# Kernel optimization log

Measured on AMD Instinct MI355X. Metric: run time of the kernel, lower is better.

## Reference

```python
import jax, jax.numpy as jnp
import numpy as np

N = 100000      # num nodes (cells)
M = 100000      # num hyperedges (hyperedge_attr has N rows, so M <= N; torch code uses max(idx1)+1)
NNZ = 3200000   # incidence entries
C = 10          # num_of_class
D_IN = 64
HID = 512


def setup_inputs() -> dict:
    key = jax.random.key(0)
    ks = jax.random.split(key, 16)
    s = 0.05
    return {
        "embedding": jax.random.normal(ks[0], (N, D_IN), jnp.float32),
        "edge_index": jax.random.randint(ks[1], (2, NNZ), 0, N, jnp.int32),
        "hyperedge_attr": jax.random.normal(ks[2], (N, D_IN), jnp.float32),
        "wq": jax.random.normal(ks[3], (D_IN, HID), jnp.float32) * s,
        "bq": jnp.zeros((HID,), jnp.float32),
        "wk": jax.random.normal(ks[4], (D_IN, HID), jnp.float32) * s,
        "bk": jnp.zeros((HID,), jnp.float32),
        "wv": jax.random.normal(ks[5], (D_IN, HID), jnp.float32) * s,
        "bv": jnp.zeros((HID,), jnp.float32),
        "wo": jax.random.normal(ks[6], (HID, D_IN), jnp.float32) * s,
        "bo": jnp.zeros((D_IN,), jnp.float32),
        "hconv_lin": jax.random.normal(ks[7], (D_IN, 1), jnp.float32) * s,
        "hconv_att": jax.random.normal(ks[8], (1, 1, 2), jnp.float32) * s,
        "hconv_bias": jnp.zeros((1,), jnp.float32),
        "head_lin": jax.random.normal(ks[9], (1, 1), jnp.float32) * s,
        "head_bias": jnp.zeros((1,), jnp.float32),
        "out_w": jax.random.normal(ks[10], (1, C), jnp.float32) * s,
        "out_b": jnp.zeros((C,), jnp.float32),
    }


def reference(embedding, edge_index, hyperedge_attr, wq, bq, wk, bk, wv, bv,
              wo, bo, hconv_lin, hconv_att, hconv_bias, head_lin, head_bias,
              out_w, out_b):
    n = embedding.shape[0]
    nnz = edge_index.shape[1]

    # ---- DualAttention over per-node sequences of length 1 ----
    x1 = embedding[:, None, :]        # [N,1,64]
    x2 = hyperedge_attr[:, None, :]   # [N,1,64]

    def sdpa(x):  # self-attention with shared Q/K/V projections
        Q = x @ wq + bq
        K = x @ wk + bk
        V = x @ wv + bv
        scores = jnp.einsum('nsd,ntd->nst', Q, K) / jnp.sqrt(jnp.float32(HID))
        return jnp.einsum('nst,ntd->nsd', jax.nn.softmax(scores, axis=-1), V)

    att_out = (sdpa(x1) + sdpa(x2)) @ wo + bo  # [N,1,64]

    idx0 = edge_index[0]  # node ids per incidence
    idx1 = edge_index[1]  # hyperedge ids per incidence

    # degree normalizations (hyperedge_weight = ones)
    ones_e = jnp.ones((nnz,), jnp.float32)
    Bdeg = jax.ops.segment_sum(ones_e, idx1, num_segments=M)  # edge size
    Binv = jnp.where(Bdeg > 0, 1.0 / Bdeg, 0.0)
    Ddeg = jax.ops.segment_sum(ones_e, idx0, num_segments=n)  # node degree
    Dinv = jnp.where(Ddeg > 0, 1.0 / Ddeg, 0.0)

    def hconv_propagate(xnode, alpha):
        # xnode: [N,H,F]; node -> edge then edge -> node, with degree norms
        m1 = Binv[idx1][:, None, None] * xnode[idx0]
        if alpha is not None:
            m1 = alpha[:, :, None] * m1
        ef = jax.ops.segment_sum(m1, idx1, num_segments=M)     # [M,H,F]
        m2 = Dinv[idx0][:, None, None] * ef[idx1]
        if alpha is not None:
            m2 = alpha[:, :, None] * m2
        return jax.ops.segment_sum(m2, idx0, num_segments=n)   # [N,H,F]

    # ---- HypergraphConv(64,1, use_attention=True), heads=1, out=1 ----
    xl = jnp.einsum('nsd,df->nsf', att_out, hconv_lin)            # [N,1,1]
    el = (hyperedge_attr @ hconv_lin)[:, :, None]                 # [N,1,1]
    alpha = (xl[idx0][:, :, 0] * hconv_att[0, :, 0] +
             el[idx1][:, :, 0] * hconv_att[0, :, 1])              # [nnz,1]
    alpha = jax.nn.leaky_relu(alpha, 0.2)
    # softmax grouped by hyperedge id (attention_mode='node')
    amax = jax.ops.segment_max(alpha, idx1, num_segments=M)
    aexp = jnp.exp(alpha - amax[idx1])
    asum = jax.ops.segment_sum(aexp, idx1, num_segments=M)
    alpha = aexp / asum[idx1]

    h = hconv_propagate(xl, alpha).reshape(n, 1) + hconv_bias     # [N,1]

    # ---- head conv: HypergraphConv(1,1), no attention ----
    hl = (h @ head_lin)[:, :, None]                               # [N,1,1]
    out = hconv_propagate(hl, None).reshape(n, 1) + head_bias     # [N,1]

    emb = jax.nn.relu(out)
    return emb @ out_w + out_b                                    # [N,C]
```

## Files before the change

### kernel.cpp

```cpp
#include <hip/hip_runtime.h>

#define M_SEG    100000
#define LOCW     256
#define LOG_LOCW 8
#define CAP      8832
#define NBS      391
#define NBT      782
#define BINB     512
#define BINT     512
#define CAPR     16
#define NROUND   2

#define FPS  4398046511104.f
#define FPSI 2.2737367544323206e-13

typedef float v4f __attribute__((ext_vector_type(4)));

__device__ __forceinline__ float edge_e(float xv, float ev, float a0, float a1) {
    float a = xv * a0 + ev * a1;
    a = a > 0.f ? a : 0.2f * a;
    return __expf(a);
}

__device__ __forceinline__ void fxadd(unsigned long long* p, float v) {
    atomicAdd(p, (unsigned long long)(long long)(v * FPS));
}
__device__ __forceinline__ float fxget(unsigned long long v) {
    return (float)((double)(long long)v * FPSI);
}

__global__ void prep_kernel(const float* __restrict__ wv, const float* __restrict__ bv,
                            const float* __restrict__ wo, const float* __restrict__ bo,
                            const float* __restrict__ hlin,
                            float* __restrict__ w_eff, float* __restrict__ c_eff) {
    __shared__ float wol[512];
    __shared__ float hl_s[64];
    __shared__ float part[512];
    __shared__ float cpart[512];
    int t = threadIdx.x;
    if (t < 64) hl_s[t] = hlin[t];
    __syncthreads();
    {
        float s = 0.f;
        for (int j = 0; j < 64; ++j) s += wo[t * 64 + j] * hl_s[j];
        wol[t] = s;
    }
    __syncthreads();
    {
        int d = t & 63, kseg = t >> 6;
        float s = 0.f;
        for (int k = kseg * 64; k < kseg * 64 + 64; ++k) s += wv[d * 512 + k] * wol[k];
        part[t] = s;
        float cs = 0.f;
        for (int k = kseg * 64; k < kseg * 64 + 64; ++k) cs += 2.f * bv[k] * wol[k];
        cpart[t] = cs;
    }
    __syncthreads();
    if (t < 64) {
        float s = 0.f;
        for (int r = 0; r < 8; ++r) s += part[r * 64 + t];
        w_eff[t] = s;
    }
    if (t == 64) {
        float s = 0.f;
        for (int r = 0; r < 512; ++r) s += cpart[r];
        for (int j = 0; j < 64; ++j) s += bo[j] * hl_s[j];
        *c_eff = s;
    }
}

__global__ void node1_kernel(const v4f* __restrict__ emb, const v4f* __restrict__ hattr,
                             const v4f* __restrict__ w_eff4, const v4f* __restrict__ hlin4,
                             const float* __restrict__ c_eff,
                             float* __restrict__ xl, float* __restrict__ el, int n) {
    int gtid = blockIdx.x * blockDim.x + threadIdx.x;
    int wave = gtid >> 6;
    int lane = threadIdx.x & 63;
    int sub  = lane >> 4;
    int q    = lane & 15;
    int node = wave * 4 + sub;
    if (node >= n) return;
    size_t base = (size_t)node * 16 + q;
    v4f ha = __builtin_nontemporal_load(hattr + base);
    v4f em = __builtin_nontemporal_load(emb + base);
    v4f w  = w_eff4[q];
    v4f h  = hlin4[q];
    float v1 = (em[0] + ha[0]) * w[0] + (em[1] + ha[1]) * w[1] +
               (em[2] + ha[2]) * w[2] + (em[3] + ha[3]) * w[3];
    float v2 = ha[0] * h[0] + ha[1] * h[1] + ha[2] * h[2] + ha[3] * h[3];
    for (int off = 8; off >= 1; off >>= 1) {
        v1 += __shfl_xor(v1, off);
        v2 += __shfl_xor(v2, off);
    }
    if (q == 0) { xl[node] = v1 + *c_eff; el[node] = v2; }
}

__global__ void hist_kernel(const int* __restrict__ idx0, const int* __restrict__ idx1,
                            unsigned* __restrict__ hist, long long nnz) {
    __shared__ unsigned h[NBT];
    for (int i = threadIdx.x; i < NBT; i += BINT) h[i] = 0u;
    __syncthreads();
    long long chunk = (nnz + BINB - 1) / BINB;
    long long e0 = (long long)blockIdx.x * chunk;
    long long e1 = e0 + chunk; if (e1 > nnz) e1 = nnz;
    for (long long e = e0 + threadIdx.x; e < e1; e += BINT) {
        int i1 = __builtin_nontemporal_load(idx1 + e);
        int i0 = __builtin_nontemporal_load(idx0 + e);
        atomicAdd(&h[i1 >> LOG_LOCW], 1u);
        atomicAdd(&h[NBS + (i0 >> LOG_LOCW)], 1u);
    }
    __syncthreads();
    for (int i = threadIdx.x; i < NBT; i += BINT)
        hist[(size_t)i * BINB + blockIdx.x] = h[i];
}

__global__ void scan_kernel(const unsigned* __restrict__ hist, unsigned* __restrict__ offs,
                            unsigned* __restrict__ cnt) {
    int gb = blockIdx.x;
    int lane = threadIdx.x;
    unsigned running = 0;
    unsigned base = (unsigned)gb * CAP;
    for (int c = 0; c < BINB; c += 64) {
        unsigned v = hist[(size_t)gb * BINB + c + lane];
        unsigned s = v;
        for (int off = 1; off < 64; off <<= 1) {
            unsigned t = __shfl_up(s, off);
            if (lane >= off) s += t;
        }
        offs[(size_t)gb * BINB + c + lane] = base + running + (s - v);
        running += __shfl(s, 63);
    }
    if (lane == 0) cnt[gb] = running;
}

__global__ void scat_kernel(const int* __restrict__ idx0, const int* __restrict__ idx1,
                            const unsigned* __restrict__ offs,
                            unsigned* __restrict__ recs, long long nnz) {
    __shared__ unsigned base_s[NBT];
    __shared__ unsigned cum_s[NBT];
    __shared__ unsigned alloc_s[NBT];
    __shared__ unsigned stage[NBT][CAPR];
    for (int i = threadIdx.x; i < NBT; i += BINT) {
        base_s[i] = offs[(size_t)i * BINB + blockIdx.x];
        cum_s[i]  = 0u;
    }
    long long chunk = (nnz + BINB - 1) / BINB;
    long long e0 = (long long)blockIdx.x * chunk;
    long long e1 = e0 + chunk; if (e1 > nnz) e1 = nnz;
    long long rchunk = (chunk + NROUND - 1) / NROUND;

    for (int rd = 0; rd < NROUND; ++rd) {
        __syncthreads();
        for (int i = threadIdx.x; i < NBT; i += BINT) alloc_s[i] = 0u;
        __syncthreads();
        long long r0 = e0 + (long long)rd * rchunk;
        long long r1 = r0 + rchunk; if (r1 > e1) r1 = e1;
        long long e = r0 + threadIdx.x;
        for (; e + 3LL * BINT < r1; e += 4LL * BINT) {
            int i0v[4], i1v[4];
            #pragma unroll
            for (int u = 0; u < 4; ++u) {
                i0v[u] = __builtin_nontemporal_load(idx0 + e + (long long)u * BINT);
                i1v[u] = __builtin_nontemporal_load(idx1 + e + (long long)u * BINT);
            }
            #pragma unroll
            for (int u = 0; u < 4; ++u) {
                int i0 = i0v[u], i1 = i1v[u];
                {
                    int b = i1 >> LOG_LOCW;
                    unsigned rec = ((unsigned)i0 << LOG_LOCW) | (unsigned)(i1 & (LOCW - 1));
                    unsigned s = atomicAdd(&alloc_s[b], 1u);
                    if (s < CAPR) stage[b][s] = rec;
                    else {
                        unsigned pos = base_s[b] + cum_s[b] + s;
                        if (pos < (unsigned)(b + 1) * CAP) recs[pos] = rec;
                    }
                }
                {
                    int b = NBS + (i0 >> LOG_LOCW);
                    unsigned rec = ((unsigned)i1 << LOG_LOCW) | (unsigned)(i0 & (LOCW - 1));
                    unsigned s = atomicAdd(&alloc_s[b], 1u);
                    if (s < CAPR) stage[b][s] = rec;
                    else {
                        unsigned pos = base_s[b] + cum_s[b] + s;
                        if (pos < (unsigned)(b + 1) * CAP) recs[pos] = rec;
                    }
                }
            }
        }
        for (; e < r1; e += BINT) {
            int i0 = __builtin_nontemporal_load(idx0 + e);
            int i1 = __builtin_nontemporal_load(idx1 + e);
            {
                int b = i1 >> LOG_LOCW;
                unsigned rec = ((unsigned)i0 << LOG_LOCW) | (unsigned)(i1 & (LOCW - 1));
                unsigned s = atomicAdd(&alloc_s[b], 1u);
                if (s < CAPR) stage[b][s] = rec;
                else {
                    unsigned pos = base_s[b] + cum_s[b] + s;
                    if (pos < (unsigned)(b + 1) * CAP) recs[pos] = rec;
                }
            }
            {
                int b = NBS + (i0 >> LOG_LOCW);
                unsigned rec = ((unsigned)i1 << LOG_LOCW) | (unsigned)(i0 & (LOCW - 1));
                unsigned s = atomicAdd(&alloc_s[b], 1u);
                if (s < CAPR) stage[b][s] = rec;
                else {
                    unsigned pos = base_s[b] + cum_s[b] + s;
                    if (pos < (unsigned)(b + 1) * CAP) recs[pos] = rec;
                }
            }
        }
        __syncthreads();
        {
            int r = threadIdx.x & (CAPR - 1);
            for (int b = threadIdx.x / CAPR; b < NBT; b += BINT / CAPR) {
                unsigned a = alloc_s[b]; if (a > CAPR) a = CAPR;
                if (r < a) {
                    unsigned pos = base_s[b] + cum_s[b] + r;
                    if (pos < (unsigned)(b + 1) * CAP) recs[pos] = stage[b][r];
                }
            }
        }
        __syncthreads();
        for (int i = threadIdx.x; i < NBT; i += BINT) cum_s[i] += alloc_s[i];
    }
}

__global__ void p1r_kernel(const unsigned* __restrict__ recs, const unsigned* __restrict__ cnt,
                           const float* __restrict__ xl, const float* __restrict__ el,
                           const float* __restrict__ hatt,
                           float* __restrict__ Binv, float2* __restrict__ elt2, int m_tot) {
    int b = blockIdx.x;
    __shared__ unsigned long long As[LOCW], Ex[LOCW];
    __shared__ unsigned Bc[LOCW];
    __shared__ float el_loc[LOCW];
    int t = threadIdx.x;
    if (t < LOCW) {
        As[t] = 0ull; Ex[t] = 0ull; Bc[t] = 0u;
        int m = (b << LOG_LOCW) + t;
        el_loc[t] = (m < m_tot) ? el[m] : 0.f;
    }
    __syncthreads();
    float a0 = hatt[0], a1 = hatt[1];
    unsigned c = cnt[b]; if (c > CAP) c = CAP;
    const unsigned* bp = recs + (size_t)b * CAP;
    unsigned k = t;
    for (; k + 7u * 512u < c; k += 8u * 512u) {
        unsigned r[8]; float xv[8];
        #pragma unroll
        for (int u = 0; u < 8; ++u) r[u] = bp[k + u * 512u];
        #pragma unroll
        for (int u = 0; u < 8; ++u) xv[u] = xl[r[u] >> LOG_LOCW];
        #pragma unroll
        for (int u = 0; u < 8; ++u) {
            int l = r[u] & (LOCW - 1);
            float ee = edge_e(xv[u], el_loc[l], a0, a1);
            fxadd(&As[l], ee);
            fxadd(&Ex[l], ee * xv[u]);
            atomicAdd(&Bc[l], 1u);
        }
    }
    for (; k < c; k += 512u) {
        unsigned rec = bp[k];
        int l = rec & (LOCW - 1);
        float xv = xl[rec >> LOG_LOCW];
        float ee = edge_e(xv, el_loc[l], a0, a1);
        fxadd(&As[l], ee);
        fxadd(&Ex[l], ee * xv);
        atomicAdd(&Bc[l], 1u);
    }
    __syncthreads();
    if (t < LOCW) {
        int m = (b << LOG_LOCW) + t;
        if (m < m_tot) {
            unsigned bd = Bc[t];
            float as = fxget(As[t]);
            float ex = fxget(Ex[t]);
            Binv[m] = bd ? 1.f / (float)bd : 0.f;
            float tv = bd ? ex / ((float)bd * as * as) : 0.f;
            elt2[m] = make_float2(el_loc[t], tv);
        }
    }
}

__global__ void p2r_kernel(const unsigned* __restrict__ recs, const unsigned* __restrict__ cnt,
                           const float* __restrict__ xl, const float2* __restrict__ elt2,
                           const float* __restrict__ hatt,
                           const float* __restrict__ hbias, const float* __restrict__ headlin,
                           float* __restrict__ hl, float* __restrict__ Dinv, int n) {
    int b = blockIdx.x;
    int gb = NBS + b;
    __shared__ unsigned long long Hs[LOCW];
    __shared__ unsigned Dc[LOCW];
    __shared__ float xl_loc[LOCW];
    int t = threadIdx.x;
    if (t < LOCW) {
        Hs[t] = 0ull; Dc[t] = 0u;
        int i = (b << LOG_LOCW) + t;
        xl_loc[t] = (i < n) ? xl[i] : 0.f;
    }
    __syncthreads();
    float a0 = hatt[0], a1 = hatt[1];
    unsigned c = cnt[gb]; if (c > CAP) c = CAP;
    const unsigned* bp = recs + (size_t)gb * CAP;
    unsigned k = t;
    for (; k + 7u * 512u < c; k += 8u * 512u) {
        unsigned r[8]; float2 et[8];
        #pragma unroll
        for (int u = 0; u < 8; ++u) r[u] = bp[k + u * 512u];
        #pragma unroll
        for (int u = 0; u < 8; ++u) et[u] = elt2[r[u] >> LOG_LOCW];
        #pragma unroll
        for (int u = 0; u < 8; ++u) {
            int l = r[u] & (LOCW - 1);
            float ee = edge_e(xl_loc[l], et[u].x, a0, a1);
            fxadd(&Hs[l], ee * et[u].y);
            atomicAdd(&Dc[l], 1u);
        }
    }
    for (; k < c; k += 512u) {
        unsigned rec = bp[k];
        int l = rec & (LOCW - 1);
        float2 et = elt2[rec >> LOG_LOCW];
        float ee = edge_e(xl_loc[l], et.x, a0, a1);
        fxadd(&Hs[l], ee * et.y);
        atomicAdd(&Dc[l], 1u);
    }
    __syncthreads();
    if (t < LOCW) {
        int i = (b << LOG_LOCW) + t;
        if (i < n) {
            unsigned dd = Dc[t];
            float dinv = dd ? 1.f / (float)dd : 0.f;
            Dinv[i] = dinv;
            hl[i] = (dinv * fxget(Hs[t]) + hbias[0]) * headlin[0];
        }
    }
}

__global__ void p3r_kernel(const unsigned* __restrict__ recs, const unsigned* __restrict__ cnt,
                           const float* __restrict__ hl, const float* __restrict__ Binv,
                           float* __restrict__ ef2b, int m_tot) {
    int b = blockIdx.x;
    __shared__ unsigned long long Es[LOCW];
    int t = threadIdx.x;
    if (t < LOCW) Es[t] = 0ull;
    __syncthreads();
    unsigned c = cnt[b]; if (c > CAP) c = CAP;
    const unsigned* bp = recs + (size_t)b * CAP;
    unsigned k = t;
    for (; k + 7u * 512u < c; k += 8u * 512u) {
        unsigned r[8]; float hv[8];
        #pragma unroll
        for (int u = 0; u < 8; ++u) r[u] = bp[k + u * 512u];
        #pragma unroll
        for (int u = 0; u < 8; ++u) hv[u] = hl[r[u] >> LOG_LOCW];
        #pragma unroll
        for (int u = 0; u < 8; ++u) fxadd(&Es[r[u] & (LOCW - 1)], hv[u]);
    }
    for (; k < c; k += 512u) {
        unsigned rec = bp[k];
        fxadd(&Es[rec & (LOCW - 1)], hl[rec >> LOG_LOCW]);
    }
    __syncthreads();
    if (t < LOCW) {
        int m = (b << LOG_LOCW) + t;
        if (m < m_tot) ef2b[m] = fxget(Es[t]) * Binv[m];
    }
}

__global__ void p4r_kernel(const unsigned* __restrict__ recs, const unsigned* __restrict__ cnt,
                           const float* __restrict__ ef2b, const float* __restrict__ Dinv,
                           const float* __restrict__ headbias,
                           const float* __restrict__ out_w, const float* __restrict__ out_b,
                           float* __restrict__ out, int n, int C) {
    int b = blockIdx.x;
    int gb = NBS + b;
    __shared__ unsigned long long Os[LOCW];
    __shared__ float r_loc[LOCW];
    int t = threadIdx.x;
    if (t < LOCW) Os[t] = 0ull;
    __syncthreads();
    unsigned c = cnt[gb]; if (c > CAP) c = CAP;
    const unsigned* bp = recs + (size_t)gb * CAP;
    unsigned k = t;
    for (; k + 7u * 512u < c; k += 8u * 512u) {
        unsigned r[8]; float ev[8];
        #pragma unroll
        for (int u = 0; u < 8; ++u) r[u] = bp[k + u * 512u];
        #pragma unroll
        for (int u = 0; u < 8; ++u) ev[u] = ef2b[r[u] >> LOG_LOCW];
        #pragma unroll
        for (int u = 0; u < 8; ++u) fxadd(&Os[r[u] & (LOCW - 1)], ev[u]);
    }
    for (; k < c; k += 512u) {
        unsigned rec = bp[k];
        fxadd(&Os[rec & (LOCW - 1)], ef2b[rec >> LOG_LOCW]);
    }
    __syncthreads();
    if (t < LOCW) {
        int i = (b << LOG_LOCW) + t;
        float o = (i < n) ? Dinv[i] * fxget(Os[t]) + headbias[0] : 0.f;
        r_loc[t] = o > 0.f ? o : 0.f;
    }
    __syncthreads();
    int total = LOCW * C;
    for (int idx = t; idx < total; idx += 512) {
        int il = idx / C, cc = idx - il * C;
        int i = (b << LOG_LOCW) + il;
        if (i < n) out[(size_t)i * C + cc] = r_loc[il] * out_w[cc] + out_b[cc];
    }
}

__global__ void f_node1(const float* __restrict__ emb, const float* __restrict__ hattr,
                        const float* __restrict__ w_eff, const float* __restrict__ hlin,
                        const float* __restrict__ c_eff,
                        float* __restrict__ xl, float* __restrict__ el, int n) {
    int wid = (int)((blockIdx.x * (long long)blockDim.x + threadIdx.x) >> 6);
    int lane = threadIdx.x & 63;
    if (wid >= n) return;
    size_t base = (size_t)wid * 64 + lane;
    float ha = hattr[base];
    float eh = emb[base] + ha;
    float v1 = eh * w_eff[lane];
    float v2 = ha * hlin[lane];
    for (int off = 32; off > 0; off >>= 1) {
        v1 += __shfl_xor(v1, off);
        v2 += __shfl_xor(v2, off);
    }
    if (lane == 0) { xl[wid] = v1 + *c_eff; el[wid] = v2; }
}
__global__ void f_p1(const int* __restrict__ idx0, const int* __restrict__ idx1,
                     const float* __restrict__ xl, const float* __restrict__ el,
                     const float* __restrict__ hatt,
                     float* __restrict__ B, float* __restrict__ D,
                     float* __restrict__ A, float* __restrict__ E, long long nnz) {
    float a0 = hatt[0], a1 = hatt[1];
    long long stride = (long long)gridDim.x * blockDim.x;
    for (long long e = blockIdx.x * (long long)blockDim.x + threadIdx.x; e < nnz; e += stride) {
        int i0 = idx0[e], i1 = idx1[e];
        float xv = xl[i0];
        float ee = edge_e(xv, el[i1], a0, a1);
        atomicAdd(&B[i1], 1.f); atomicAdd(&D[i0], 1.f);
        atomicAdd(&A[i1], ee);  atomicAdd(&E[i1], ee * xv);
    }
}
__global__ void f_r1m(const float* __restrict__ B, const float* __restrict__ A,
                      const float* __restrict__ E,
                      float* __restrict__ Binv, float* __restrict__ t, int m) {
    int i = blockIdx.x * blockDim.x + threadIdx.x;
    if (i >= m) return;
    float bd = B[i];
    Binv[i] = bd > 0.f ? 1.f / bd : 0.f;
    t[i]    = bd > 0.f ? E[i] / (bd * A[i] * A[i]) : 0.f;
}
__global__ void f_r1n(const float* __restrict__ D, float* __restrict__ Dinv, int n) {
    int i = blockIdx.x * blockDim.x + threadIdx.x;
    if (i < n) { float dd = D[i]; Dinv[i] = dd > 0.f ? 1.f / dd : 0.f; }
}
__global__ void f_p2(const int* __restrict__ idx0, const int* __restrict__ idx1,
                     const float* __restrict__ xl, const float* __restrict__ el,
                     const float* __restrict__ hatt, const float* __restrict__ t,
                     float* __restrict__ H, long long nnz) {
    float a0 = hatt[0], a1 = hatt[1];
    long long stride = (long long)gridDim.x * blockDim.x;
    for (long long e = blockIdx.x * (long long)blockDim.x + threadIdx.x; e < nnz; e += stride) {
        int i0 = idx0[e], i1 = idx1[e];
        float ee = edge_e(xl[i0], el[i1], a0, a1);
        atomicAdd(&H[i0], ee * t[i1]);
    }
}
__global__ void f_r2(const float* __restrict__ H, const float* __restrict__ Dinv,
                     const float* __restrict__ hbias, const float* __restrict__ headlin,
                     float* __restrict__ hl, int n) {
    int i = blockIdx.x * blockDim.x + threadIdx.x;
    if (i < n) hl[i] = (Dinv[i] * H[i] + hbias[0]) * headlin[0];
}
__global__ void f_p3(const int* __restrict__ idx0, const int* __restrict__ idx1,
                     const float* __restrict__ hl, float* __restrict__ E2, long long nnz) {
    long long stride = (long long)gridDim.x * blockDim.x;
    for (long long e = blockIdx.x * (long long)blockDim.x + threadIdx.x; e < nnz; e += stride)
        atomicAdd(&E2[idx1[e]], hl[idx0[e]]);
}
__global__ void f_r3(const float* __restrict__ E2, const float* __restrict__ Binv,
                     float* __restrict__ ef2b, int m) {
    int i = blockIdx.x * blockDim.x + threadIdx.x;
    if (i < m) ef2b[i] = E2[i] * Binv[i];
}
__global__ void f_p4(const int* __restrict__ idx0, const int* __restrict__ idx1,
                     const float* __restrict__ ef2b, float* __restrict__ O, long long nnz) {
    long long stride = (long long)gridDim.x * blockDim.x;
    for (long long e = blockIdx.x * (long long)blockDim.x + threadIdx.x; e < nnz; e += stride)
        atomicAdd(&O[idx0[e]], ef2b[idx1[e]]);
}
__global__ void f_out(const float* __restrict__ O, const float* __restrict__ Dinv,
                      const float* __restrict__ headbias,
                      const float* __restrict__ out_w, const float* __restrict__ out_b,
                      float* __restrict__ out, int n, int C) {
    int i = blockIdx.x * blockDim.x + threadIdx.x;
    if (i >= n) return;
    float o = Dinv[i] * O[i] + headbias[0];
    float r = o > 0.f ? o : 0.f;
    for (int c = 0; c < C; ++c) out[(size_t)i * C + c] = r * out_w[c] + out_b[c];
}

extern "C" void kernel_launch(void* const* d_in, const int* in_sizes, int n_in,
                              void* d_out, int out_size, void* d_ws, size_t ws_size,
                              hipStream_t stream) {
    const float* emb     = (const float*)d_in[0];
    const int*   eidx    = (const int*)  d_in[1];
    const float* hattr   = (const float*)d_in[2];
    const float* wv      = (const float*)d_in[7];
    const float* bv      = (const float*)d_in[8];
    const float* wo      = (const float*)d_in[9];
    const float* bo      = (const float*)d_in[10];
    const float* hlin    = (const float*)d_in[11];
    const float* hatt    = (const float*)d_in[12];
    const float* hbias   = (const float*)d_in[13];
    const float* headlin = (const float*)d_in[14];
    const float* headbias= (const float*)d_in[15];
    const float* out_w   = (const float*)d_in[16];
    const float* out_b   = (const float*)d_in[17];

    int n = in_sizes[0] / 64;
    long long nnz = in_sizes[1] / 2;
    int C = in_sizes[16];
    const int M = M_SEG;
    const int* idx0 = eidx;
    const int* idx1 = eidx + nnz;

    size_t need_words = 2 * (size_t)NBT * BINB
                      + NBT
                      + (size_t)NBT * CAP
                      + 8 * (size_t)n + 80;
    bool ok = (ws_size >= need_words * sizeof(unsigned)) && (n == 100000);

    float* ws = (float*)d_ws;

    if (ok) {
        unsigned* hist = (unsigned*)ws;
        unsigned* offs = hist + (size_t)NBT * BINB;
        unsigned* cnt  = offs + (size_t)NBT * BINB;
        unsigned* recs = cnt + NBT;
        float2* elt2 = (float2*)(recs + (size_t)NBT * CAP);
        float* xl    = (float*)(elt2 + n);
        float* el    = xl + n;
        float* Binv  = el + n;
        float* Dinv  = Binv + M;
        float* hl    = Dinv + n;
        float* ef2b  = hl + n;
        float* w_eff = ef2b + M;
        float* c_eff = w_eff + 64;

        prep_kernel<<<1, 512, 0, stream>>>(wv, bv, wo, bo, hlin, w_eff, c_eff);
        int n1_blocks = ((n + 3) / 4 + 3) / 4;
        node1_kernel<<<n1_blocks, 256, 0, stream>>>((const v4f*)emb, (const v4f*)hattr,
                                                    (const v4f*)w_eff, (const v4f*)hlin,
                                                    c_eff, xl, el, n);

        hist_kernel<<<BINB, BINT, 0, stream>>>(idx0, idx1, hist, nnz);
        scan_kernel<<<NBT, 64, 0, stream>>>(hist, offs, cnt);
        scat_kernel<<<BINB, BINT, 0, stream>>>(idx0, idx1, offs, recs, nnz);

        p1r_kernel<<<NBS, 512, 0, stream>>>(recs, cnt, xl, el, hatt, Binv, elt2, M);
        p2r_kernel<<<NBS, 512, 0, stream>>>(recs, cnt, xl, elt2, hatt, hbias, headlin,
                                            hl, Dinv, n);
        p3r_kernel<<<NBS, 512, 0, stream>>>(recs, cnt, hl, Binv, ef2b, M);
        p4r_kernel<<<NBS, 512, 0, stream>>>(recs, cnt, ef2b, Dinv, headbias, out_w, out_b,
                                            (float*)d_out, n, C);
    } else {
        float* B    = ws;
        float* D    = B + M;
        float* A    = D + n;
        float* E    = A + M;
        float* H    = E + M;
        float* E2   = H + n;
        float* O    = E2 + M;
        float* zend = O + n;
        float* xl    = zend;
        float* el    = xl + n;
        float* Binv  = el + n;
        float* tbuf  = Binv + M;
        float* Dinv  = tbuf + M;
        float* hl    = Dinv + n;
        float* ef2b  = hl + n;
        float* w_eff = ef2b + M;
        float* c_eff = w_eff + 64;

        hipMemsetAsync(d_ws, 0, (size_t)(zend - ws) * sizeof(float), stream);
        prep_kernel<<<1, 512, 0, stream>>>(wv, bv, wo, bo, hlin, w_eff, c_eff);
        f_node1<<<(n + 3) / 4, 256, 0, stream>>>(emb, hattr, w_eff, hlin, c_eff, xl, el, n);

        const int EG = 2048, EB = 256;
        int mg = (M + 255) / 256, ng = (n + 255) / 256;
        f_p1<<<EG, EB, 0, stream>>>(idx0, idx1, xl, el, hatt, B, D, A, E, nnz);
        f_r1m<<<mg, 256, 0, stream>>>(B, A, E, Binv, tbuf, M);
        f_r1n<<<ng, 256, 0, stream>>>(D, Dinv, n);
        f_p2<<<EG, EB, 0, stream>>>(idx0, idx1, xl, el, hatt, tbuf, H, nnz);
        f_r2<<<ng, 256, 0, stream>>>(H, Dinv, hbias, headlin, hl, n);
        f_p3<<<EG, EB, 0, stream>>>(idx0, idx1, hl, E2, nnz);
        f_r3<<<mg, 256, 0, stream>>>(E2, Binv, ef2b, M);
        f_p4<<<EG, EB, 0, stream>>>(idx0, idx1, ef2b, O, nnz);
        f_out<<<ng, 256, 0, stream>>>(O, Dinv, headbias, out_w, out_b, (float*)d_out, n, C);
    }
}
```

Baseline: 157.9 us.

## Merge launch pairs and pack degree counts into fixed-point LDS atomics

Fuses the weight-prep kernel into the histogram launch as an extra block, and fuses the node projection with the per-bucket scan into one launch, removing two kernel launches and their serialization gaps. In p1r and p2r the separate degree-count LDS atomic is removed: the count is packed into the top 12 bits of the 64-bit fixed-point accumulator, using 41 fractional bits and adding a +2 bias for signed values in p2r. This halves LDS atomics in those passes but narrows fixed-point range and precision, and caps the per-slot count field at 4095.

```diff
diff --git a/kernel.cpp b/kernel.cpp
--- a/kernel.cpp
+++ b/kernel.cpp
@@ -11,8 +11,12 @@
 #define CAPR     16
 #define NROUND   2
 
-#define FPS  4398046511104.f
-#define FPSI 2.2737367544323206e-13
+#define FPS42  4398046511104.f
+#define FPSI42 2.2737367544323206e-13
+#define FPS41  2199023255552.f
+#define FPSI41 4.547473508864641e-13
+#define MASK52 ((1ULL << 52) - 1ULL)
+#define CNT1   (1ULL << 52)
 
 typedef float v4f __attribute__((ext_vector_type(4)));
 
@@ -22,115 +26,118 @@
     return __expf(a);
 }
 
-__device__ __forceinline__ void fxadd(unsigned long long* p, float v) {
-    atomicAdd(p, (unsigned long long)(long long)(v * FPS));
-}
-__device__ __forceinline__ float fxget(unsigned long long v) {
-    return (float)((double)(long long)v * FPSI);
-}
-
-__global__ void prep_kernel(const float* __restrict__ wv, const float* __restrict__ bv,
-                            const float* __restrict__ wo, const float* __restrict__ bo,
-                            const float* __restrict__ hlin,
-                            float* __restrict__ w_eff, float* __restrict__ c_eff) {
+__device__ __forceinline__ void fxadd42(unsigned long long* p, float v) {
+    atomicAdd(p, (unsigned long long)(long long)(v * FPS42));
+}
+__device__ __forceinline__ float fxget42(unsigned long long v) {
+    return (float)((double)(long long)v * FPSI42);
+}
+
+__global__ void histprep_kernel(const int* __restrict__ idx0, const int* __restrict__ idx1,
+                                unsigned* __restrict__ hist, long long nnz,
+                                const float* __restrict__ wv, const float* __restrict__ bv,
+                                const float* __restrict__ wo, const float* __restrict__ bo,
+                                const float* __restrict__ hlin,
+                                float* __restrict__ w_eff, float* __restrict__ c_eff) {
+    __shared__ unsigned h[NBT];
     __shared__ float wol[512];
     __shared__ float hl_s[64];
     __shared__ float part[512];
     __shared__ float cpart[512];
     int t = threadIdx.x;
-    if (t < 64) hl_s[t] = hlin[t];
-    __syncthreads();
-    {
-        float s = 0.f;
-        for (int j = 0; j < 64; ++j) s += wo[t * 64 + j] * hl_s[j];
-        wol[t] = s;
-    }
-    __syncthreads();
-    {
-        int d = t & 63, kseg = t >> 6;
-        float s = 0.f;
-        for (int k = kseg * 64; k < kseg * 64 + 64; ++k) s += wv[d * 512 + k] * wol[k];
-        part[t] = s;
-        float cs = 0.f;
-        for (int k = kseg * 64; k < kseg * 64 + 64; ++k) cs += 2.f * bv[k] * wol[k];
-        cpart[t] = cs;
-    }
-    __syncthreads();
-    if (t < 64) {
-        float s = 0.f;
-        for (int r = 0; r < 8; ++r) s += part[r * 64 + t];
-        w_eff[t] = s;
-    }
-    if (t == 64) {
-        float s = 0.f;
-        for (int r = 0; r < 512; ++r) s += cpart[r];
-        for (int j = 0; j < 64; ++j) s += bo[j] * hl_s[j];
-        *c_eff = s;
-    }
-}
-
-__global__ void node1_kernel(const v4f* __restrict__ emb, const v4f* __restrict__ hattr,
-                             const v4f* __restrict__ w_eff4, const v4f* __restrict__ hlin4,
-                             const float* __restrict__ c_eff,
-                             float* __restrict__ xl, float* __restrict__ el, int n) {
-    int gtid = blockIdx.x * blockDim.x + threadIdx.x;
-    int wave = gtid >> 6;
-    int lane = threadIdx.x & 63;
-    int sub  = lane >> 4;
-    int q    = lane & 15;
-    int node = wave * 4 + sub;
-    if (node >= n) return;
-    size_t base = (size_t)node * 16 + q;
-    v4f ha = __builtin_nontemporal_load(hattr + base);
-    v4f em = __builtin_nontemporal_load(emb + base);
-    v4f w  = w_eff4[q];
-    v4f h  = hlin4[q];
-    float v1 = (em[0] + ha[0]) * w[0] + (em[1] + ha[1]) * w[1] +
-               (em[2] + ha[2]) * w[2] + (em[3] + ha[3]) * w[3];
-    float v2 = ha[0] * h[0] + ha[1] * h[1] + ha[2] * h[2] + ha[3] * h[3];
-    for (int off = 8; off >= 1; off >>= 1) {
-        v1 += __shfl_xor(v1, off);
-        v2 += __shfl_xor(v2, off);
-    }
-    if (q == 0) { xl[node] = v1 + *c_eff; el[node] = v2; }
-}
-
-__global__ void hist_kernel(const int* __restrict__ idx0, const int* __restrict__ idx1,
-                            unsigned* __restrict__ hist, long long nnz) {
-    __shared__ unsigned h[NBT];
-    for (int i = threadIdx.x; i < NBT; i += BINT) h[i] = 0u;
-    __syncthreads();
-    long long chunk = (nnz + BINB - 1) / BINB;
-    long long e0 = (long long)blockIdx.x * chunk;
-    long long e1 = e0 + chunk; if (e1 > nnz) e1 = nnz;
-    for (long long e = e0 + threadIdx.x; e < e1; e += BINT) {
-        int i1 = __builtin_nontemporal_load(idx1 + e);
-        int i0 = __builtin_nontemporal_load(idx0 + e);
-        atomicAdd(&h[i1 >> LOG_LOCW], 1u);
-        atomicAdd(&h[NBS + (i0 >> LOG_LOCW)], 1u);
-    }
-    __syncthreads();
-    for (int i = threadIdx.x; i < NBT; i += BINT)
-        hist[(size_t)i * BINB + blockIdx.x] = h[i];
-}
-
-__global__ void scan_kernel(const unsigned* __restrict__ hist, unsigned* __restrict__ offs,
-                            unsigned* __restrict__ cnt) {
-    int gb = blockIdx.x;
-    int lane = threadIdx.x;
-    unsigned running = 0;
-    unsigned base = (unsigned)gb * CAP;
-    for (int c = 0; c < BINB; c += 64) {
-        unsigned v = hist[(size_t)gb * BINB + c + lane];
-        unsigned s = v;
-        for (int off = 1; off < 64; off <<= 1) {
-            unsigned t = __shfl_up(s, off);
-            if (lane >= off) s += t;
-        }
-        offs[(size_t)gb * BINB + c + lane] = base + running + (s - v);
-        running += __shfl(s, 63);
-    }
-    if (lane == 0) cnt[gb] = running;
+    if (blockIdx.x < BINB) {
+        for (int i = t; i < NBT; i += BINT) h[i] = 0u;
+        __syncthreads();
+        long long chunk = (nnz + BINB - 1) / BINB;
+        long long e0 = (long long)blockIdx.x * chunk;
+        long long e1 = e0 + chunk; if (e1 > nnz) e1 = nnz;
+        for (long long e = e0 + t; e < e1; e += BINT) {
+            int i1 = __builtin_nontemporal_load(idx1 + e);
+            int i0 = __builtin_nontemporal_load(idx0 + e);
+            atomicAdd(&h[i1 >> LOG_LOCW], 1u);
+            atomicAdd(&h[NBS + (i0 >> LOG_LOCW)], 1u);
+        }
+        __syncthreads();
+        for (int i = t; i < NBT; i += BINT)
+            hist[(size_t)i * BINB + blockIdx.x] = h[i];
+    } else {
+        if (t < 64) hl_s[t] = hlin[t];
+        __syncthreads();
+        {
+            float s = 0.f;
+            for (int j = 0; j < 64; ++j) s += wo[t * 64 + j] * hl_s[j];
+            wol[t] = s;
+        }
+        __syncthreads();
+        {
+            int d = t & 63, kseg = t >> 6;
+            float s = 0.f;
+            for (int k = kseg * 64; k < kseg * 64 + 64; ++k) s += wv[d * 512 + k] * wol[k];
+            part[t] = s;
+            float cs = 0.f;
+            for (int k = kseg * 64; k < kseg * 64 + 64; ++k) cs += 2.f * bv[k] * wol[k];
+            cpart[t] = cs;
+        }
+        __syncthreads();
+        if (t < 64) {
+            float s = 0.f;
+            for (int r = 0; r < 8; ++r) s += part[r * 64 + t];
+            w_eff[t] = s;
+        }
+        if (t == 64) {
+            float s = 0.f;
+            for (int r = 0; r < 512; ++r) s += cpart[r];
+            for (int j = 0; j < 64; ++j) s += bo[j] * hl_s[j];
+            *c_eff = s;
+        }
+    }
+}
+
+__global__ void nodescan_kernel(const v4f* __restrict__ emb, const v4f* __restrict__ hattr,
+                                const v4f* __restrict__ w_eff4, const v4f* __restrict__ hlin4,
+                                const float* __restrict__ c_eff,
+                                float* __restrict__ xl, float* __restrict__ el, int n,
+                                const unsigned* __restrict__ hist, unsigned* __restrict__ offs,
+                                unsigned* __restrict__ cnt, int node1b) {
+    int t = threadIdx.x;
+    if ((int)blockIdx.x < node1b) {
+        int wave = (int)blockIdx.x * 8 + (t >> 6);
+        int lane = t & 63;
+        int sub  = lane >> 4;
+        int q    = lane & 15;
+        int node = wave * 4 + sub;
+        if (node >= n) return;
+        size_t base = (size_t)node * 16 + q;
+        v4f ha = __builtin_nontemporal_load(hattr + base);
+        v4f em = __builtin_nontemporal_load(emb + base);
+        v4f w  = w_eff4[q];
+        v4f h  = hlin4[q];
+        float v1 = (em[0] + ha[0]) * w[0] + (em[1] + ha[1]) * w[1] +
+                   (em[2] + ha[2]) * w[2] + (em[3] + ha[3]) * w[3];
+        float v2 = ha[0] * h[0] + ha[1] * h[1] + ha[2] * h[2] + ha[3] * h[3];
+        for (int off = 8; off >= 1; off >>= 1) {
+            v1 += __shfl_xor(v1, off);
+            v2 += __shfl_xor(v2, off);
+        }
+        if (q == 0) { xl[node] = v1 + *c_eff; el[node] = v2; }
+    } else {
+        int gb = ((int)blockIdx.x - node1b) * 8 + (t >> 6);
+        if (gb >= NBT) return;
+        int lane = t & 63;
+        unsigned running = 0;
+        unsigned base = (unsigned)gb * CAP;
+        for (int c = 0; c < BINB; c += 64) {
+            unsigned v = hist[(size_t)gb * BINB + c + lane];
+            unsigned s = v;
+            for (int off = 1; off < 64; off <<= 1) {
+                unsigned tt = __shfl_up(s, off);
+                if (lane >= off) s += tt;
+            }
+            offs[(size_t)gb * BINB + c + lane] = base + running + (s - v);
+            running += __shfl(s, 63);
+        }
+        if (lane == 0) cnt[gb] = running;
+    }
 }
 
 __global__ void scat_kernel(const int* __restrict__ idx0, const int* __restrict__ idx1,
@@ -234,11 +241,10 @@
                            float* __restrict__ Binv, float2* __restrict__ elt2, int m_tot) {
     int b = blockIdx.x;
     __shared__ unsigned long long As[LOCW], Ex[LOCW];
-    __shared__ unsigned Bc[LOCW];
     __shared__ float el_loc[LOCW];
     int t = threadIdx.x;
     if (t < LOCW) {
-        As[t] = 0ull; Ex[t] = 0ull; Bc[t] = 0u;
+        As[t] = 0ull; Ex[t] = 0ull;
         int m = (b << LOG_LOCW) + t;
         el_loc[t] = (m < m_tot) ? el[m] : 0.f;
     }
@@ -257,9 +263,8 @@
         for (int u = 0; u < 8; ++u) {
             int l = r[u] & (LOCW - 1);
             float ee = edge_e(xv[u], el_loc[l], a0, a1);
-            fxadd(&As[l], ee);
-            fxadd(&Ex[l], ee * xv[u]);
-            atomicAdd(&Bc[l], 1u);
+            atomicAdd(&As[l], CNT1 + (unsigned long long)(ee * FPS41));
+            fxadd42(&Ex[l], ee * xv[u]);
         }
     }
     for (; k < c; k += 512u) {
@@ -267,17 +272,17 @@
         int l = rec & (LOCW - 1);
         float xv = xl[rec >> LOG_LOCW];
         float ee = edge_e(xv, el_loc[l], a0, a1);
-        fxadd(&As[l], ee);
-        fxadd(&Ex[l], ee * xv);
-        atomicAdd(&Bc[l], 1u);
+        atomicAdd(&As[l], CNT1 + (unsigned long long)(ee * FPS41));
+        fxadd42(&Ex[l], ee * xv);
     }
     __syncthreads();
     if (t < LOCW) {
         int m = (b << LOG_LOCW) + t;
         if (m < m_tot) {
-            unsigned bd = Bc[t];
-            float as = fxget(As[t]);
-            float ex = fxget(Ex[t]);
+            unsigned long long a = As[t];
+            unsigned bd = (unsigned)(a >> 52);
+            float as = (float)((double)(a & MASK52) * FPSI41);
+            float ex = fxget42(Ex[t]);
             Binv[m] = bd ? 1.f / (float)bd : 0.f;
             float tv = bd ? ex / ((float)bd * as * as) : 0.f;
             elt2[m] = make_float2(el_loc[t], tv);
@@ -293,11 +298,10 @@
     int b = blockIdx.x;
     int gb = NBS + b;
     __shared__ unsigned long long Hs[LOCW];
-    __shared__ unsigned Dc[LOCW];
     __shared__ float xl_loc[LOCW];
     int t = threadIdx.x;
     if (t < LOCW) {
-        Hs[t] = 0ull; Dc[t] = 0u;
+        Hs[t] = 0ull;
         int i = (b << LOG_LOCW) + t;
         xl_loc[t] = (i < n) ? xl[i] : 0.f;
     }
@@ -316,8 +320,8 @@
         for (int u = 0; u < 8; ++u) {
             int l = r[u] & (LOCW - 1);
             float ee = edge_e(xl_loc[l], et[u].x, a0, a1);
-            fxadd(&Hs[l], ee * et[u].y);
-            atomicAdd(&Dc[l], 1u);
+            float v = ee * et[u].y;
+            atomicAdd(&Hs[l], CNT1 + (unsigned long long)((v + 2.0f) * FPS41));
         }
     }
     for (; k < c; k += 512u) {
@@ -325,17 +329,19 @@
         int l = rec & (LOCW - 1);
         float2 et = elt2[rec >> LOG_LOCW];
         float ee = edge_e(xl_loc[l], et.x, a0, a1);
-        fxadd(&Hs[l], ee * et.y);
-        atomicAdd(&Dc[l], 1u);
+        float v = ee * et.y;
+        atomicAdd(&Hs[l], CNT1 + (unsigned long long)((v + 2.0f) * FPS41));
     }
     __syncthreads();
     if (t < LOCW) {
         int i = (b << LOG_LOCW) + t;
         if (i < n) {
-            unsigned dd = Dc[t];
+            unsigned long long hh = Hs[t];
+            unsigned dd = (unsigned)(hh >> 52);
+            double hs = (double)(hh & MASK52) * (double)FPSI41 - 2.0 * (double)dd;
             float dinv = dd ? 1.f / (float)dd : 0.f;
             Dinv[i] = dinv;
-            hl[i] = (dinv * fxget(Hs[t]) + hbias[0]) * headlin[0];
+            hl[i] = (dinv * (float)hs + hbias[0]) * headlin[0];
         }
     }
 }
@@ -358,16 +364,16 @@
         #pragma unroll
         for (int u = 0; u < 8; ++u) hv[u] = hl[r[u] >> LOG_LOCW];
         #pragma unroll
-        for (int u = 0; u < 8; ++u) fxadd(&Es[r[u] & (LOCW - 1)], hv[u]);
+        for (int u = 0; u < 8; ++u) fxadd42(&Es[r[u] & (LOCW - 1)], hv[u]);
     }
     for (; k < c; k += 512u) {
         unsigned rec = bp[k];
-        fxadd(&Es[rec & (LOCW - 1)], hl[rec >> LOG_LOCW]);
+        fxadd42(&Es[rec & (LOCW - 1)], hl[rec >> LOG_LOCW]);
     }
     __syncthreads();
     if (t < LOCW) {
         int m = (b << LOG_LOCW) + t;
-        if (m < m_tot) ef2b[m] = fxget(Es[t]) * Binv[m];
+        if (m < m_tot) ef2b[m] = fxget42(Es[t]) * Binv[m];
     }
 }
 
@@ -393,16 +399,16 @@
         #pragma unroll
         for (int u = 0; u < 8; ++u) ev[u] = ef2b[r[u] >> LOG_LOCW];
         #pragma unroll
-        for (int u = 0; u < 8; ++u) fxadd(&Os[r[u] & (LOCW - 1)], ev[u]);
+        for (int u = 0; u < 8; ++u) fxadd42(&Os[r[u] & (LOCW - 1)], ev[u]);
     }
     for (; k < c; k += 512u) {
         unsigned rec = bp[k];
-        fxadd(&Os[rec & (LOCW - 1)], ef2b[rec >> LOG_LOCW]);
+        fxadd42(&Os[rec & (LOCW - 1)], ef2b[rec >> LOG_LOCW]);
     }
     __syncthreads();
     if (t < LOCW) {
         int i = (b << LOG_LOCW) + t;
-        float o = (i < n) ? Dinv[i] * fxget(Os[t]) + headbias[0] : 0.f;
+        float o = (i < n) ? Dinv[i] * fxget42(Os[t]) + headbias[0] : 0.f;
         r_loc[t] = o > 0.f ? o : 0.f;
     }
     __syncthreads();
@@ -414,6 +420,33 @@
     }
 }
 
+__global__ void f_prep(const float* __restrict__ wv, const float* __restrict__ bv,
+                       const float* __restrict__ wo, const float* __restrict__ bo,
+                       const float* __restrict__ hlin,
+                       float* __restrict__ w_eff, float* __restrict__ c_eff) {
+    __shared__ float wol[512];
+    __shared__ float hl_s[64];
+    int t = threadIdx.x;
+    if (t < 64) hl_s[t] = hlin[t];
+    __syncthreads();
+    {
+        float s = 0.f;
+        for (int j = 0; j < 64; ++j) s += wo[t * 64 + j] * hl_s[j];
+        wol[t] = s;
+    }
+    __syncthreads();
+    if (t < 64) {
+        float s = 0.f;
+        for (int k = 0; k < 512; ++k) s += wv[t * 512 + k] * wol[k];
+        w_eff[t] = s;
+    }
+    if (t == 64) {
+        float s = 0.f;
+        for (int k = 0; k < 512; ++k) s += 2.f * bv[k] * wol[k];
+        for (int j = 0; j < 64; ++j) s += bo[j] * hl_s[j];
+        *c_eff = s;
+    }
+}
 __global__ void f_node1(const float* __restrict__ emb, const float* __restrict__ hattr,
                         const float* __restrict__ w_eff, const float* __restrict__ hlin,
                         const float* __restrict__ c_eff,
@@ -554,14 +587,14 @@
         float* w_eff = ef2b + M;
         float* c_eff = w_eff + 64;
 
-        prep_kernel<<<1, 512, 0, stream>>>(wv, bv, wo, bo, hlin, w_eff, c_eff);
-        int n1_blocks = ((n + 3) / 4 + 3) / 4;
-        node1_kernel<<<n1_blocks, 256, 0, stream>>>((const v4f*)emb, (const v4f*)hattr,
-                                                    (const v4f*)w_eff, (const v4f*)hlin,
-                                                    c_eff, xl, el, n);
-
-        hist_kernel<<<BINB, BINT, 0, stream>>>(idx0, idx1, hist, nnz);
-        scan_kernel<<<NBT, 64, 0, stream>>>(hist, offs, cnt);
+        histprep_kernel<<<BINB + 1, BINT, 0, stream>>>(idx0, idx1, hist, nnz,
+                                                       wv, bv, wo, bo, hlin, w_eff, c_eff);
+        int node1b = (((n + 3) / 4) + 7) / 8;
+        int scanb  = (NBT + 7) / 8;
+        nodescan_kernel<<<node1b + scanb, 512, 0, stream>>>(
+            (const v4f*)emb, (const v4f*)hattr, (const v4f*)w_eff, (const v4f*)hlin,
+            c_eff, xl, el, n, hist, offs, cnt, node1b);
+
         scat_kernel<<<BINB, BINT, 0, stream>>>(idx0, idx1, offs, recs, nnz);
 
         p1r_kernel<<<NBS, 512, 0, stream>>>(recs, cnt, xl, el, hatt, Binv, elt2, M);
@@ -590,7 +623,7 @@
         float* c_eff = w_eff + 64;
 
         hipMemsetAsync(d_ws, 0, (size_t)(zend - ws) * sizeof(float), stream);
-        prep_kernel<<<1, 512, 0, stream>>>(wv, bv, wo, bo, hlin, w_eff, c_eff);
+        f_prep<<<1, 512, 0, stream>>>(wv, bv, wo, bo, hlin, w_eff, c_eff);
         f_node1<<<(n + 3) / 4, 256, 0, stream>>>(emb, hattr, w_eff, hlin, c_eff, xl, el, n);
 
         const int EG = 2048, EB = 256;
```

Result: faster. 152.6 us (-3.4%).
